# Kernel tuning notes

Hardware: AMD Instinct MI355X
Metric: run time of the kernel (lower is better)

The kernel has to match this reference:

```python
import jax, jax.numpy as jnp
import numpy as np
from jax import lax

NPOINT = 1024
K = 32
GN_GROUPS = 32
EPS = 1e-5


def farthest_point_sample(xyz, npoint):
    # xyz: (B,N,3) -> idx (B,npoint). Deterministic start at index 0.
    B, N, _ = xyz.shape
    dist0 = jnp.full((B, N), 1e10, dtype=xyz.dtype)
    far0 = jnp.zeros((B,), dtype=jnp.int32)
    barange = jnp.arange(B)

    def step(carry, _):
        dist, far = carry
        centroid = xyz[barange, far][:, None, :]              # (B,1,3)
        d = jnp.sum((xyz - centroid) ** 2, axis=-1)           # (B,N)
        dist = jnp.minimum(dist, d)
        far_new = jnp.argmax(dist, axis=-1).astype(jnp.int32)
        return (dist, far_new), far

    _, idxs = lax.scan(step, (dist0, far0), None, length=npoint)
    return idxs.T  # (B,npoint)


def conv1x1(x, w, b):
    # x: (B,Cin,M,K), w: (Cout,Cin)
    return jnp.einsum('oc,bcmk->bomk', w, x) + b[None, :, None, None]


def group_norm(x, gamma, beta, groups):
    B, C, M, Kk = x.shape
    xg = x.reshape(B, groups, C // groups, M, Kk)
    mu = xg.mean(axis=(2, 3, 4), keepdims=True)
    var = xg.var(axis=(2, 3, 4), keepdims=True)
    xg = (xg - mu) * lax.rsqrt(var + EPS)
    x = xg.reshape(B, C, M, Kk)
    return x * gamma[None, :, None, None] + beta[None, :, None, None]


def setup_inputs() -> dict:
    key = jax.random.key(0)
    ks = jax.random.split(key, 4)
    B, N, Cin = 16, 8192, 64
    hid, out_ch, in_total = 64, 128, 3 + Cin
    return {
        'xyz': jax.random.normal(ks[0], (B, N, 3), jnp.float32),
        'feat': jax.random.normal(ks[1], (B, N, Cin), jnp.float32),
        'w1': jax.random.normal(ks[2], (hid, in_total), jnp.float32) * 0.1,
        'b1': jnp.zeros((hid,), jnp.float32),
        'g1w': jnp.ones((hid,), jnp.float32),
        'g1b': jnp.zeros((hid,), jnp.float32),
        'w2': jax.random.normal(ks[3], (out_ch, hid), jnp.float32) * 0.1,
        'b2': jnp.zeros((out_ch,), jnp.float32),
        'g2w': jnp.ones((out_ch,), jnp.float32),
        'g2b': jnp.zeros((out_ch,), jnp.float32),
    }


def reference(xyz, feat, w1, b1, g1w, g1b, w2, b2, g2w, g2b):
    B, N, _ = xyz.shape
    M = min(NPOINT, N)
    k = min(K, N)

    fps_idx = farthest_point_sample(lax.stop_gradient(xyz), M)   # (B,M) ints
    batch = jnp.arange(B)[:, None]
    centroids = xyz[batch, fps_idx]                              # (B,M,3)

    # kNN via squared distances (same ordering as cdist p=2)
    d2 = (jnp.sum(centroids ** 2, -1)[:, :, None]
          + jnp.sum(xyz ** 2, -1)[:, None, :]
          - 2.0 * jnp.einsum('bmd,bnd->bmn', centroids, xyz))    # (B,M,N)
    knn_idx = lax.top_k(-d2, k)[1]                               # (B,M,k)

    b3 = jnp.arange(B)[:, None, None]
    group_xyz = xyz[b3, knn_idx]                                 # (B,M,k,3)
    delta = group_xyz - centroids[:, :, None, :]
    gfeat = feat[b3, knn_idx]                                    # (B,M,k,Cin)
    gf = jnp.concatenate([delta, gfeat], axis=-1)                # (B,M,k,3+Cin)
    x = jnp.transpose(gf, (0, 3, 1, 2))                          # (B,C,M,k)

    x = jax.nn.relu(group_norm(conv1x1(x, w1, b1), g1w, g1b, GN_GROUPS))
    x = jax.nn.relu(group_norm(conv1x1(x, w2, b2), g2w, g2b, GN_GROUPS))
    out = jnp.max(x, axis=-1)                                    # (B,out_ch,M)
    new_feat = jnp.transpose(out, (0, 2, 1))                     # (B,M,out_ch)
    return (centroids, new_feat)
```

## Files before the change

### kernel.cpp

```cpp
#include <hip/hip_runtime.h>
#include <cstdint>

#define BB 16
#define NN 8192
#define MM 1024
#define KNN 32
#define CIN 64
#define HID 64
#define OCH 128

#define KNN_OFF   0u
#define SUM1_OFF  524288u
#define SUM2_OFF  526336u
#define A1_OFF    530432u
#define D1_OFF    531456u
#define A2_OFF    532480u
#define D2_OFF    534528u
#define W2B_OFF   536576u
#define W1B_OFF   540672u
#define Y1_OFF    543744u
#define PTS4_OFF  Y1_OFF

typedef unsigned long long u64;
typedef float f32x4 __attribute__((ext_vector_type(4)));
typedef float f32x2 __attribute__((ext_vector_type(2)));
typedef short bf16x8 __attribute__((ext_vector_type(8)));

__device__ __forceinline__ unsigned short f2bf(float f) {
  union { float f; unsigned u; } v; v.f = f;
  unsigned r = v.u + 0x7FFFu + ((v.u >> 16) & 1u);
  return (unsigned short)(r >> 16);
}

__global__ __launch_bounds__(256) void k0_init(const float* __restrict__ xyz,
                                               const float* __restrict__ w1,
                                               const float* __restrict__ w2,
                                               float* __restrict__ ws) {
  int t = blockIdx.x * 256 + threadIdx.x;
  if (t < 12288) ws[SUM1_OFF + t] = 0.0f;
  if (t < 4096) {
    unsigned lo = f2bf(w2[2 * t]);
    unsigned hi = f2bf(w2[2 * t + 1]);
    ((unsigned*)(ws + W2B_OFF))[t] = lo | (hi << 16);
  }
  if (t < 6144) {
    int n = t / 96, kk = t % 96;
    float val = 0.0f;
    if (kk < 3) val = w1[n * 67 + kk];
    else if (kk >= 4 && kk < 68) val = w1[n * 67 + kk - 1];
    ((unsigned short*)(ws + W1B_OFF))[t] = f2bf(val);
  }
  if (t < BB * NN) {
    #pragma clang fp contract(off)
    float x = xyz[(size_t)t * 3], y = xyz[(size_t)t * 3 + 1], z = xyz[(size_t)t * 3 + 2];
    ((float4*)(ws + PTS4_OFF))[t] = make_float4(x, y, z, (x * x + y * y) + z * z);
  }
}

__device__ __forceinline__ u64 wave_max_u64(u64 v) {
  #define DPP_RND(ctrl, rm)                                                     \
  {                                                                             \
    int lo_ = __builtin_amdgcn_update_dpp(0, (int)(unsigned)(v & 0xFFFFFFFFull),\
                                          ctrl, rm, 0xf, true);                 \
    int hi_ = __builtin_amdgcn_update_dpp(0, (int)(unsigned)(v >> 32),          \
                                          ctrl, rm, 0xf, true);                 \
    u64 o_ = ((u64)(unsigned)hi_ << 32) | (unsigned)lo_;                        \
    v = o_ > v ? o_ : v;                                                        \
  }
  DPP_RND(0x111, 0xf)
  DPP_RND(0x112, 0xf)
  DPP_RND(0x114, 0xf)
  DPP_RND(0x118, 0xf)
  DPP_RND(0x142, 0xa)
  DPP_RND(0x143, 0xc)
  #undef DPP_RND
  return v;
}

__global__ __launch_bounds__(256) void fps_kernel(const float* __restrict__ xyz,
                                                  float* __restrict__ cent) {
  #pragma clang fp contract(off)
  __shared__ float4 sp4[NN];
  __shared__ u64 slots[MM];
  const int b = blockIdx.x, tid = threadIdx.x;
  const float* xp = xyz + (size_t)b * NN * 3;
  f32x2 px[16], py[16], pz[16];
  float dist0[16], dist1[16];
  #pragma unroll
  for (int i = 0; i < 16; ++i) {
    int n0 = tid + (2 * i) * 256, n1 = tid + (2 * i + 1) * 256;
    float x0 = xp[n0 * 3], y0 = xp[n0 * 3 + 1], z0 = xp[n0 * 3 + 2];
    float x1 = xp[n1 * 3], y1 = xp[n1 * 3 + 1], z1 = xp[n1 * 3 + 2];
    px[i] = (f32x2){x0, x1}; py[i] = (f32x2){y0, y1}; pz[i] = (f32x2){z0, z1};
    sp4[n0] = make_float4(x0, y0, z0, 0.0f);
    sp4[n1] = make_float4(x1, y1, z1, 0.0f);
    dist0[i] = 1e10f; dist1[i] = 1e10f;
  }
  for (int s = tid; s < MM; s += 256) slots[s] = 0ull;
  __syncthreads();
  int far = 0;
  for (int step = 0; step < MM; ++step) {
    float4 c4 = sp4[far];
    f32x2 cx = (f32x2){c4.x, c4.x}, cy = (f32x2){c4.y, c4.y}, cz = (f32x2){c4.z, c4.z};
    float best = -1.0f; int bi = 0;
    #pragma unroll
    for (int i = 0; i < 16; ++i) {
      f32x2 dx = px[i] - cx, dy = py[i] - cy, dz = pz[i] - cz;
      f32x2 d = (dx * dx + dy * dy) + dz * dz;
      float dm0 = fminf(dist0[i], d.x);
      float dm1 = fminf(dist1[i], d.y);
      dist0[i] = dm0; dist1[i] = dm1;
      if (dm0 > best) { best = dm0; bi = tid + (2 * i) * 256; }
      if (dm1 > best) { best = dm1; bi = tid + (2 * i + 1) * 256; }
    }
    u64 key = ((u64)__float_as_uint(best) << 32) | (unsigned)(8191 - bi);
    key = wave_max_u64(key);
    if ((tid & 63) == 63) atomicMax(&slots[step], key);
    __syncthreads();
    far = 8191 - (int)(unsigned)(slots[step] & 0xFFFFFFFFull);
  }
  float* co = cent + (size_t)b * MM * 3;
  for (int s = tid; s < MM; s += 256) {
    int fs = (s == 0) ? 0 : (8191 - (int)(unsigned)(slots[s - 1] & 0xFFFFFFFFull));
    float4 c = sp4[fs];
    co[s * 3 + 0] = c.x; co[s * 3 + 1] = c.y; co[s * 3 + 2] = c.z;
  }
}

__global__ __launch_bounds__(512) void knn_kernel(const float4* __restrict__ pts4,
                                                  const float* __restrict__ cent,
                                                  int* __restrict__ knnout) {
  #pragma clang fp contract(off)
  __shared__ __align__(16) char smem[65536];
  unsigned* blo = (unsigned*)smem;
  unsigned* bhi = (unsigned*)(smem + 32768);
  u64* marea = (u64*)smem;
  const int tid = threadIdx.x;
  const int lane = tid & 63;
  const int w = tid >> 6;
  const int b = blockIdx.x >> 4;
  const int m = ((blockIdx.x & 15) << 6) + lane;
  const float* cp = cent + ((size_t)b * MM + m) * 3;
  float cx = cp[0], cy = cp[1], cz = cp[2];
  float cn2 = (cx * cx + cy * cy) + cz * cz;
  u64 key[32];
  {
    u64 initk = ((u64)(__float_as_uint(3e38f) ^ 0x80000000u) << 32) | 0xFFFFFFFFull;
    #pragma unroll
    for (int j = 0; j < 32; ++j) key[j] = initk;
  }
  float kthf = 3e38f;

  auto insert = [&](u64 cand) {
    bool cprev = false; u64 kprev = 0;
    #pragma unroll
    for (int j = 0; j < 32; ++j) {
      bool cj = cand < key[j];
      u64 cur = key[j];
      u64 nv = cj ? cand : cur;
      key[j] = cprev ? kprev : nv;
      cprev = cj; kprev = cur;
    }
    unsigned hb = (unsigned)(key[31] >> 32);
    unsigned ob = (hb & 0x80000000u) ? (hb ^ 0x80000000u) : ~hb;
    kthf = __uint_as_float(ob);
  };

  int cnt = 0;
  auto flush = [&]() {
    int mc = cnt;
    #pragma unroll
    for (int off = 1; off < 64; off <<= 1) { int o = __shfl_xor(mc, off); mc = o > mc ? o : mc; }
    for (int i = 0; i < mc; ++i) {
      u64 cand = ((u64)bhi[i * 512 + tid] << 32) | blo[i * 512 + tid];
      if (i < cnt && cand < key[31]) insert(cand);
    }
    cnt = 0;
  };

  const int nbase = __builtin_amdgcn_readfirstlane(w * 1024);
  const float4* pb = pts4 + (size_t)b * NN + nbase;
  for (int n0 = 0; n0 < 1024; n0 += 8) {
    #pragma unroll
    for (int j = 0; j < 8; ++j) {
      int n = n0 + j;
      float4 p = pb[n];
      float dot = fmaf(cz, p.z, fmaf(cy, p.y, cx * p.x));
      float d2 = (cn2 + p.w) - 2.0f * dot;
      if (d2 <= kthf) {
        unsigned db = __float_as_uint(d2);
        unsigned fk = db ^ (((int)db < 0) ? 0xFFFFFFFFu : 0x80000000u);
        blo[cnt * 512 + tid] = (unsigned)(nbase + n);
        bhi[cnt * 512 + tid] = fk;
        cnt++;
      }
    }
    if (__ballot(cnt >= 9)) flush();
  }
  flush();
  __syncthreads();

  auto publish = [&](int a) {
    u64* ap = marea + a * 2048;
    #pragma unroll
    for (int j = 0; j < 32; ++j) ap[j * 64 + lane] = key[j];
  };
  auto merge_from = [&](int a) {
    u64* ap = marea + a * 2048;
    for (int j = 0; j < 32; ++j) {
      u64 cand = ap[j * 64 + lane];
      if (cand < key[31]) insert(cand);
    }
  };
  if (w & 1) publish(w >> 1);
  __syncthreads();
  if (!(w & 1)) merge_from(w >> 1);
  __syncthreads();
  if (w == 2) publish(0);
  if (w == 6) publish(1);
  __syncthreads();
  if (w == 0) merge_from(0);
  if (w == 4) merge_from(1);
  __syncthreads();
  if (w == 4) publish(0);
  __syncthreads();
  if (w == 0) {
    merge_from(0);
    int* op = knnout + ((size_t)b * MM + m) * KNN;
    #pragma unroll
    for (int j = 0; j < 32; ++j) op[j] = (int)(key[j] & 0xFFFFFFFFull);
  }
}

__global__ __launch_bounds__(256) void conv1_kernel(const float* __restrict__ xyz,
                                                    const float* __restrict__ feat,
                                                    const float* __restrict__ cent,
                                                    const int* __restrict__ knn,
                                                    const unsigned short* __restrict__ w1b,
                                                    const float* __restrict__ b1,
                                                    float* __restrict__ y1,
                                                    float* __restrict__ sums1) {
  __shared__ __align__(16) unsigned short gsm[4][32 * 104];
  __shared__ float s1acc[64], q1acc[64];
  const int tid = threadIdx.x, lane = tid & 63, w = tid >> 6;
  const int wid = blockIdx.x * 4 + w;
  const int b = wid >> 10;
  unsigned short* gf = gsm[w];

  if (tid < 64) { s1acc[tid] = 0.0f; q1acc[tid] = 0.0f; }
  __syncthreads();

  int idxv = 0;
  if (lane < 32) idxv = knn[(size_t)wid * 32 + lane];

  {
    int row = lane >> 1, h = (lane & 1) * 16;
    ushort4 z4 = {0, 0, 0, 0};
    *(ushort4*)(gf + row * 104 + 64 + h + 0)  = z4;
    *(ushort4*)(gf + row * 104 + 64 + h + 4)  = z4;
    *(ushort4*)(gf + row * 104 + 64 + h + 8)  = z4;
    *(ushort4*)(gf + row * 104 + 64 + h + 12) = z4;
  }
  const float* cp = cent + (size_t)wid * 3;
  float ccx = cp[0], ccy = cp[1], ccz = cp[2];
  if (lane < 32) {
    const float* pp = xyz + ((size_t)b * NN + idxv) * 3;
    ushort4 dv;
    dv.x = f2bf(pp[0] - ccx); dv.y = f2bf(pp[1] - ccy); dv.z = f2bf(pp[2] - ccz);
    dv.w = 0;
    *(ushort4*)(gf + lane * 104) = dv;
  }
  const float4* fb = (const float4*)feat;
  #pragma unroll
  for (int i = 0; i < 8; ++i) {
    int v = i * 64 + lane;
    int row = v >> 4, part = v & 15;
    int ridx = __shfl(idxv, row);
    float4 f4 = fb[(size_t)(b * NN + ridx) * 16 + part];
    ushort4 s;
    s.x = f2bf(f4.x); s.y = f2bf(f4.y); s.z = f2bf(f4.z); s.w = f2bf(f4.w);
    *(ushort4*)(gf + row * 104 + 4 + part * 4) = s;
  }
  __builtin_amdgcn_s_waitcnt(0);
  __builtin_amdgcn_wave_barrier();

  const int quad = lane >> 4, lr = lane & 15;
  bf16x8 bw[4][3];
  float b1v[4];
  #pragma unroll
  for (int nt = 0; nt < 4; ++nt) {
    #pragma unroll
    for (int ks = 0; ks < 3; ++ks)
      bw[nt][ks] = *(const bf16x8*)(w1b + (size_t)(nt * 16 + lr) * 96 + ks * 32 + quad * 8);
    b1v[nt] = b1[nt * 16 + lr];
  }
  f32x4 acc[2][4];
  #pragma unroll
  for (int mt = 0; mt < 2; ++mt)
    #pragma unroll
    for (int nt = 0; nt < 4; ++nt)
      acc[mt][nt] = (f32x4){0.f, 0.f, 0.f, 0.f};
  #pragma unroll
  for (int ks = 0; ks < 3; ++ks) {
    bf16x8 a0 = *(const bf16x8*)(gf + (0 + lr) * 104 + ks * 32 + quad * 8);
    bf16x8 a1 = *(const bf16x8*)(gf + (16 + lr) * 104 + ks * 32 + quad * 8);
    #pragma unroll
    for (int nt = 0; nt < 4; ++nt) {
      acc[0][nt] = __builtin_amdgcn_mfma_f32_16x16x32_bf16(a0, bw[nt][ks], acc[0][nt], 0, 0, 0);
      acc[1][nt] = __builtin_amdgcn_mfma_f32_16x16x32_bf16(a1, bw[nt][ks], acc[1][nt], 0, 0, 0);
    }
  }
  float* yo = y1 + (size_t)wid * 2048;
  float s_nt[4] = {0.f, 0.f, 0.f, 0.f};
  float q_nt[4] = {0.f, 0.f, 0.f, 0.f};
  #pragma unroll
  for (int mt = 0; mt < 2; ++mt)
    #pragma unroll
    for (int rg = 0; rg < 4; ++rg) {
      int row = mt * 16 + quad * 4 + rg;
      #pragma unroll
      for (int nt = 0; nt < 4; ++nt) {
        float z = acc[mt][nt][rg] + b1v[nt];
        yo[row * 64 + nt * 16 + lr] = z;
        s_nt[nt] += z;
        q_nt[nt] = fmaf(z, z, q_nt[nt]);
      }
    }
  #pragma unroll
  for (int nt = 0; nt < 4; ++nt) {
    float s = s_nt[nt], q = q_nt[nt];
    s += __shfl_xor(s, 16); s += __shfl_xor(s, 32);
    q += __shfl_xor(q, 16); q += __shfl_xor(q, 32);
    if (quad == 0) {
      atomicAdd(&s1acc[nt * 16 + lr], s);
      atomicAdd(&q1acc[nt * 16 + lr], q);
    }
  }
  __syncthreads();
  if (tid < 64) {
    atomicAdd(&sums1[b * 128 + tid], s1acc[tid]);
    atomicAdd(&sums1[b * 128 + 64 + tid], q1acc[tid]);
  }
}

__global__ void coeffs_kernel(const float* __restrict__ sums,
                              const float* __restrict__ gamma,
                              const float* __restrict__ beta,
                              float* __restrict__ a, float* __restrict__ d,
                              int nch, int cpg, float invn) {
  int t = blockIdx.x * blockDim.x + threadIdx.x;
  if (t >= BB * nch) return;
  int b = t / nch, c = t % nch, g = c / cpg;
  float S = 0, Q = 0;
  for (int j = 0; j < cpg; ++j) {
    S += sums[b * 2 * nch + g * cpg + j];
    Q += sums[b * 2 * nch + nch + g * cpg + j];
  }
  float mu = S * invn;
  float var = Q * invn - mu * mu;
  float rs = 1.0f / sqrtf(var + 1e-5f);
  float ga = gamma[c];
  a[t] = rs * ga;
  d[t] = beta[c] - mu * rs * ga;
}

struct Conv2Frag {
  bf16x8 bfr[8][2];
  float  b2v[8];
};

__device__ __forceinline__ void load_w2_frags(const unsigned short* __restrict__ w2b,
                                              const float* __restrict__ b2,
                                              int lane, Conv2Frag& F) {
  const int quad = lane >> 4, lr = lane & 15;
  #pragma unroll
  for (int nt = 0; nt < 8; ++nt) {
    #pragma unroll
    for (int t = 0; t < 2; ++t)
      F.bfr[nt][t] = *(const bf16x8*)(w2b + (size_t)(nt * 16 + lr) * 64 + t * 32 + quad * 8);
    F.b2v[nt] = b2[nt * 16 + lr];
  }
}

__device__ __forceinline__ void conv2_wave_mfma(const float* __restrict__ y1,
                                                const float* __restrict__ a1,
                                                const float* __restrict__ d1,
                                                unsigned short* __restrict__ hrow,
                                                int wid, int b, int lane,
                                                const Conv2Frag& F,
                                                f32x4 acc[2][8]) {
  const int quad = lane >> 4, lr = lane & 15;
  const int r = lane >> 1, c0 = (lane & 1) * 32;
  const float4* yrow = (const float4*)(y1 + (size_t)wid * 2048 + r * 64 + c0);
  const float4* ap = (const float4*)(a1 + b * 64 + c0);
  const float4* dp = (const float4*)(d1 + b * 64 + c0);
  #pragma unroll
  for (int g = 0; g < 8; ++g) {
    float4 v = yrow[g];
    float4 av = ap[g & 7], dv = dp[g & 7];
    ushort4 sv;
    sv.x = f2bf(fmaxf(0.0f, fmaf(v.x, av.x, dv.x)));
    sv.y = f2bf(fmaxf(0.0f, fmaf(v.y, av.y, dv.y)));
    sv.z = f2bf(fmaxf(0.0f, fmaf(v.z, av.z, dv.z)));
    sv.w = f2bf(fmaxf(0.0f, fmaf(v.w, av.w, dv.w)));
    *(ushort4*)(hrow + r * 72 + c0 + 4 * g) = sv;
  }
  __builtin_amdgcn_s_waitcnt(0);
  __builtin_amdgcn_wave_barrier();
  #pragma unroll
  for (int mt = 0; mt < 2; ++mt)
    #pragma unroll
    for (int nt = 0; nt < 8; ++nt)
      acc[mt][nt] = (f32x4){0.f, 0.f, 0.f, 0.f};
  #pragma unroll
  for (int t = 0; t < 2; ++t) {
    bf16x8 a0 = *(const bf16x8*)(hrow + (0 + lr) * 72 + t * 32 + quad * 8);
    bf16x8 a1f = *(const bf16x8*)(hrow + (16 + lr) * 72 + t * 32 + quad * 8);
    #pragma unroll
    for (int nt = 0; nt < 8; ++nt) {
      acc[0][nt] = __builtin_amdgcn_mfma_f32_16x16x32_bf16(a0,  F.bfr[nt][t], acc[0][nt], 0, 0, 0);
      acc[1][nt] = __builtin_amdgcn_mfma_f32_16x16x32_bf16(a1f, F.bfr[nt][t], acc[1][nt], 0, 0, 0);
    }
  }
}

__global__ __launch_bounds__(256) void conv2_stats_kernel(const float* __restrict__ y1,
                                                          const float* __restrict__ a1,
                                                          const float* __restrict__ d1,
                                                          const unsigned short* __restrict__ w2b,
                                                          const float* __restrict__ b2,
                                                          float* __restrict__ sums2) {
  __shared__ __align__(16) unsigned short hsm[4][32 * 72];
  __shared__ float sacc[128], qacc[128];
  const int tid = threadIdx.x, lane = tid & 63, w = tid >> 6;
  const int wid = blockIdx.x * 4 + w;
  const int b = blockIdx.x >> 8;
  if (tid < 128) { sacc[tid] = 0.0f; qacc[tid] = 0.0f; }
  __syncthreads();
  Conv2Frag F;
  load_w2_frags(w2b, b2, lane, F);
  f32x4 acc[2][8];
  conv2_wave_mfma(y1, a1, d1, hsm[w], wid, b, lane, F, acc);
  const int lr = lane & 15;
  #pragma unroll
  for (int nt = 0; nt < 8; ++nt) {
    float s = 0, q = 0;
    #pragma unroll
    for (int mt = 0; mt < 2; ++mt)
      #pragma unroll
      for (int rg = 0; rg < 4; ++rg) {
        float z = acc[mt][nt][rg] + F.b2v[nt];
        s += z; q = fmaf(z, z, q);
      }
    atomicAdd(&sacc[nt * 16 + lr], s);
    atomicAdd(&qacc[nt * 16 + lr], q);
  }
  __syncthreads();
  if (tid < 128) {
    atomicAdd(&sums2[b * 256 + tid], sacc[tid]);
    atomicAdd(&sums2[b * 256 + 128 + tid], qacc[tid]);
  }
}

__global__ __launch_bounds__(256) void final_kernel(const float* __restrict__ y1,
                                                    const float* __restrict__ a1,
                                                    const float* __restrict__ d1,
                                                    const unsigned short* __restrict__ w2b,
                                                    const float* __restrict__ b2,
                                                    const float* __restrict__ a2,
                                                    const float* __restrict__ d2,
                                                    float* __restrict__ nf) {
  __shared__ __align__(16) unsigned short hsm[4][32 * 72];
  const int tid = threadIdx.x, lane = tid & 63, w = tid >> 6;
  const int wid = blockIdx.x * 4 + w;
  const int b = blockIdx.x >> 8;
  Conv2Frag F;
  load_w2_frags(w2b, b2, lane, F);
  f32x4 acc[2][8];
  conv2_wave_mfma(y1, a1, d1, hsm[w], wid, b, lane, F, acc);
  const int lr = lane & 15;
  float az[8], dz[8];
  #pragma unroll
  for (int nt = 0; nt < 8; ++nt) {
    az[nt] = a2[b * 128 + nt * 16 + lr];
    dz[nt] = d2[b * 128 + nt * 16 + lr];
  }
  float pmax[8];
  #pragma unroll
  for (int nt = 0; nt < 8; ++nt) {
    float mx = -3e38f;
    #pragma unroll
    for (int mt = 0; mt < 2; ++mt)
      #pragma unroll
      for (int rg = 0; rg < 4; ++rg) {
        float z = acc[mt][nt][rg] + F.b2v[nt];
        float v = fmaxf(0.0f, fmaf(z, az[nt], dz[nt]));
        mx = fmaxf(mx, v);
      }
    mx = fmaxf(mx, __shfl_xor(mx, 16));
    mx = fmaxf(mx, __shfl_xor(mx, 32));
    pmax[nt] = mx;
  }
  if (lane < 16) {
    float* op = nf + (size_t)wid * 128;
    #pragma unroll
    for (int nt = 0; nt < 8; ++nt) op[nt * 16 + lr] = pmax[nt];
  }
}

extern "C" void kernel_launch(void* const* d_in, const int* in_sizes, int n_in,
                              void* d_out, int out_size, void* d_ws, size_t ws_size,
                              hipStream_t stream) {
  const float* xyz  = (const float*)d_in[0];
  const float* feat = (const float*)d_in[1];
  const float* w1   = (const float*)d_in[2];
  const float* b1   = (const float*)d_in[3];
  const float* g1w  = (const float*)d_in[4];
  const float* g1b  = (const float*)d_in[5];
  const float* w2   = (const float*)d_in[6];
  const float* b2   = (const float*)d_in[7];
  const float* g2w  = (const float*)d_in[8];
  const float* g2b  = (const float*)d_in[9];
  float* ws = (float*)d_ws;
  float* cent = (float*)d_out;
  float* nf   = (float*)d_out + BB * MM * 3;
  const float4* pts4 = (const float4*)(ws + PTS4_OFF);
  int*   knn   = (int*)(ws + KNN_OFF);
  float* sums1 = ws + SUM1_OFF;
  float* sums2 = ws + SUM2_OFF;
  float* a1 = ws + A1_OFF; float* d1 = ws + D1_OFF;
  float* a2 = ws + A2_OFF; float* d2 = ws + D2_OFF;
  const unsigned short* w2b = (const unsigned short*)(ws + W2B_OFF);
  const unsigned short* w1b = (const unsigned short*)(ws + W1B_OFF);
  float* y1 = ws + Y1_OFF;

  hipLaunchKernelGGL(k0_init, dim3(512), dim3(256), 0, stream, xyz, w1, w2, ws);
  hipLaunchKernelGGL(fps_kernel, dim3(16), dim3(256), 0, stream, xyz, cent);
  hipLaunchKernelGGL(knn_kernel, dim3(256), dim3(512), 0, stream, pts4, cent, knn);
  hipLaunchKernelGGL(conv1_kernel, dim3(4096), dim3(256), 0, stream,
                     xyz, feat, cent, knn, w1b, b1, y1, sums1);
  hipLaunchKernelGGL(coeffs_kernel, dim3(4), dim3(256), 0, stream,
                     sums1, g1w, g1b, a1, d1, 64, 2, 1.0f / 65536.0f);
  hipLaunchKernelGGL(conv2_stats_kernel, dim3(4096), dim3(256), 0, stream,
                     y1, a1, d1, w2b, b2, sums2);
  hipLaunchKernelGGL(coeffs_kernel, dim3(8), dim3(256), 0, stream,
                     sums2, g2w, g2b, a2, d2, 128, 4, 1.0f / 131072.0f);
  hipLaunchKernelGGL(final_kernel, dim3(4096), dim3(256), 0, stream,
                     y1, a1, d1, w2b, b2, a2, d2, nf);
}
```

Baseline: 1.548 ms.

## Replace final conv2 recompute with per-channel max/min and monotone affine select

The stats pass now also computes, for each output channel, the max and min of the pre-norm conv2 output over the 32 neighbours. It writes them into the wave's own y1 scratch region, which is no longer needed after the read. A lightweight elementwise kernel then applies relu(a*z+d), choosing max or min by the sign of the group-norm scale a. This removes a second full conv2 pass (y1 reload plus MFMA) in exchange for overwriting y1 in place and relying on the monotonicity of the affine-plus-relu map.

```diff
diff --git a/kernel.cpp b/kernel.cpp
--- a/kernel.cpp
+++ b/kernel.cpp
@@ -424,7 +424,7 @@
   }
 }
 
-__global__ __launch_bounds__(256) void conv2_stats_kernel(const float* __restrict__ y1,
+__global__ __launch_bounds__(256) void conv2_stats_kernel(float* __restrict__ y1,
                                                           const float* __restrict__ a1,
                                                           const float* __restrict__ d1,
                                                           const unsigned short* __restrict__ w2b,
@@ -442,18 +442,31 @@
   f32x4 acc[2][8];
   conv2_wave_mfma(y1, a1, d1, hsm[w], wid, b, lane, F, acc);
   const int lr = lane & 15;
+  float zmx[8], zmn[8];
   #pragma unroll
   for (int nt = 0; nt < 8; ++nt) {
-    float s = 0, q = 0;
+    float s = 0, q = 0, mx = -3e38f, mn = 3e38f;
     #pragma unroll
     for (int mt = 0; mt < 2; ++mt)
       #pragma unroll
       for (int rg = 0; rg < 4; ++rg) {
         float z = acc[mt][nt][rg] + F.b2v[nt];
         s += z; q = fmaf(z, z, q);
+        mx = fmaxf(mx, z); mn = fminf(mn, z);
       }
     atomicAdd(&sacc[nt * 16 + lr], s);
     atomicAdd(&qacc[nt * 16 + lr], q);
+    mx = fmaxf(mx, __shfl_xor(mx, 16)); mx = fmaxf(mx, __shfl_xor(mx, 32));
+    mn = fminf(mn, __shfl_xor(mn, 16)); mn = fminf(mn, __shfl_xor(mn, 32));
+    zmx[nt] = mx; zmn[nt] = mn;
+  }
+  if (lane < 16) {
+    float* zp = y1 + (size_t)wid * 2048;
+    #pragma unroll
+    for (int nt = 0; nt < 8; ++nt) {
+      zp[nt * 16 + lr] = zmx[nt];
+      zp[128 + nt * 16 + lr] = zmn[nt];
+    }
   }
   __syncthreads();
   if (tid < 128) {
@@ -462,50 +475,19 @@
   }
 }
 
-__global__ __launch_bounds__(256) void final_kernel(const float* __restrict__ y1,
-                                                    const float* __restrict__ a1,
-                                                    const float* __restrict__ d1,
-                                                    const unsigned short* __restrict__ w2b,
-                                                    const float* __restrict__ b2,
-                                                    const float* __restrict__ a2,
-                                                    const float* __restrict__ d2,
-                                                    float* __restrict__ nf) {
-  __shared__ __align__(16) unsigned short hsm[4][32 * 72];
-  const int tid = threadIdx.x, lane = tid & 63, w = tid >> 6;
-  const int wid = blockIdx.x * 4 + w;
-  const int b = blockIdx.x >> 8;
-  Conv2Frag F;
-  load_w2_frags(w2b, b2, lane, F);
-  f32x4 acc[2][8];
-  conv2_wave_mfma(y1, a1, d1, hsm[w], wid, b, lane, F, acc);
-  const int lr = lane & 15;
-  float az[8], dz[8];
-  #pragma unroll
-  for (int nt = 0; nt < 8; ++nt) {
-    az[nt] = a2[b * 128 + nt * 16 + lr];
-    dz[nt] = d2[b * 128 + nt * 16 + lr];
-  }
-  float pmax[8];
-  #pragma unroll
-  for (int nt = 0; nt < 8; ++nt) {
-    float mx = -3e38f;
-    #pragma unroll
-    for (int mt = 0; mt < 2; ++mt)
-      #pragma unroll
-      for (int rg = 0; rg < 4; ++rg) {
-        float z = acc[mt][nt][rg] + F.b2v[nt];
-        float v = fmaxf(0.0f, fmaf(z, az[nt], dz[nt]));
-        mx = fmaxf(mx, v);
-      }
-    mx = fmaxf(mx, __shfl_xor(mx, 16));
-    mx = fmaxf(mx, __shfl_xor(mx, 32));
-    pmax[nt] = mx;
-  }
-  if (lane < 16) {
-    float* op = nf + (size_t)wid * 128;
-    #pragma unroll
-    for (int nt = 0; nt < 8; ++nt) op[nt * 16 + lr] = pmax[nt];
-  }
+__global__ __launch_bounds__(256) void final_lite(const float* __restrict__ y1,
+                                                  const float* __restrict__ a2,
+                                                  const float* __restrict__ d2,
+                                                  float* __restrict__ nf) {
+  int idx = blockIdx.x * 256 + threadIdx.x;
+  int wid = idx >> 7, c = idx & 127;
+  int b = wid >> 10;
+  const float* zp = y1 + (size_t)wid * 2048;
+  float zmx = zp[c];
+  float zmn = zp[128 + c];
+  float az = a2[b * 128 + c], dz = d2[b * 128 + c];
+  float z = (az >= 0.0f) ? zmx : zmn;
+  nf[(size_t)wid * 128 + c] = fmaxf(0.0f, fmaf(z, az, dz));
 }
 
 extern "C" void kernel_launch(void* const* d_in, const int* in_sizes, int n_in,
@@ -545,6 +527,6 @@
                      y1, a1, d1, w2b, b2, sums2);
   hipLaunchKernelGGL(coeffs_kernel, dim3(8), dim3(256), 0, stream,
                      sums2, g2w, g2b, a2, d2, 128, 4, 1.0f / 131072.0f);
-  hipLaunchKernelGGL(final_kernel, dim3(4096), dim3(256), 0, stream,
-                     y1, a1, d1, w2b, b2, a2, d2, nf);
-}
+  hipLaunchKernelGGL(final_lite, dim3(8192), dim3(256), 0, stream,
+                     y1, a2, d2, nf);
+}
```

Measured after the change: 1.494 ms. 1.04x faster.
